# Kernel optimization log

Hardware: AMD Instinct MI355X
Metric: run time of the kernel (lower is better)

Reference implementation:

```python
import jax, jax.numpy as jnp
import numpy as np

DIM = 1024
HEADS = 16
HEAD_DIM = DIM // HEADS
SCALE = HEAD_DIM ** -0.5
HIDDEN = 4 * DIM
EPS = 1e-5


def _ln(x, g, b):
    m = jnp.mean(x, -1, keepdims=True)
    v = jnp.mean(jnp.square(x - m), -1, keepdims=True)
    return (x - m) / jnp.sqrt(v + EPS) * g + b


def _attn(x, wqkv, qb, vb, wp, bp):
    # x: (B, N, C). qkv bias = concat(q_bias, zeros, v_bias) as in the torch code.
    B, N, C = x.shape
    bias = jnp.concatenate([qb, jnp.zeros_like(vb), vb])
    qkv = (x @ wqkv.T + bias).reshape(B, N, 3, HEADS, HEAD_DIM).transpose(2, 0, 3, 1, 4)
    q, k, v = qkv[0], qkv[1], qkv[2]
    # qk_float=True: logits computed in float32
    logits = jnp.einsum('bhqd,bhkd->bhqk', (q * SCALE).astype(jnp.float32), k.astype(jnp.float32))
    a = jax.nn.softmax(logits, axis=-1).astype(x.dtype)
    o = jnp.einsum('bhqk,bhkd->bqhd', a, v).reshape(B, N, C)
    return o @ wp.T + bp


def setup_inputs() -> dict:
    key = jax.random.key(0)
    ks = jax.random.split(key, 16)
    s = 0.02
    d = {
        'x': jax.random.normal(ks[0], (4, 8, 196, DIM), jnp.float32),
        'cls_token': jax.random.normal(ks[1], (4, DIM), jnp.float32),
        # temporal branch
        'tln_g': jnp.ones((DIM,), jnp.float32), 'tln_b': jnp.zeros((DIM,), jnp.float32),
        't_wqkv': jax.random.normal(ks[2], (3 * DIM, DIM), jnp.float32) * s,
        't_qb': jax.random.normal(ks[3], (DIM,), jnp.float32) * s,
        't_vb': jax.random.normal(ks[4], (DIM,), jnp.float32) * s,
        't_wproj': jax.random.normal(ks[5], (DIM, DIM), jnp.float32) * s,
        't_bproj': jnp.zeros((DIM,), jnp.float32),
        't_fc_w': jax.random.normal(ks[6], (DIM, DIM), jnp.float32) * s,
        't_fc_b': jnp.zeros((DIM,), jnp.float32),
        # spatial branch
        'n1_g': jnp.ones((DIM,), jnp.float32), 'n1_b': jnp.zeros((DIM,), jnp.float32),
        's_wqkv': jax.random.normal(ks[7], (3 * DIM, DIM), jnp.float32) * s,
        's_qb': jax.random.normal(ks[8], (DIM,), jnp.float32) * s,
        's_vb': jax.random.normal(ks[9], (DIM,), jnp.float32) * s,
        's_wproj': jax.random.normal(ks[10], (DIM, DIM), jnp.float32) * s,
        's_bproj': jnp.zeros((DIM,), jnp.float32),
        # mlp
        'n2_g': jnp.ones((DIM,), jnp.float32), 'n2_b': jnp.zeros((DIM,), jnp.float32),
        'fc1_w': jax.random.normal(ks[11], (HIDDEN, DIM), jnp.float32) * s,
        'fc1_b': jnp.zeros((HIDDEN,), jnp.float32),
        'fc2_w': jax.random.normal(ks[12], (DIM, HIDDEN), jnp.float32) * s,
        'fc2_b': jnp.zeros((DIM,), jnp.float32),
    }
    return d


def reference(x, cls_token, tln_g, tln_b, t_wqkv, t_qb, t_vb, t_wproj, t_bproj,
              t_fc_w, t_fc_b, n1_g, n1_b, s_wqkv, s_qb, s_vb, s_wproj, s_bproj,
              n2_g, n2_b, fc1_w, fc1_b, fc2_w, fc2_b):
    B, T, N, C = x.shape
    # temporal attention: 'b t n m -> (b n) t m'
    xt = x.transpose(0, 2, 1, 3).reshape(B * N, T, C)
    xt = _attn(_ln(xt, tln_g, tln_b), t_wqkv, t_qb, t_vb, t_wproj, t_bproj)
    # '(b n) t m -> b (n t) m'
    xt = xt.reshape(B, N * T, C)
    xt = xt @ t_fc_w.T + t_fc_b
    xt = x.transpose(0, 2, 1, 3).reshape(B, N * T, C) + xt
    # spatial attention with cls token per frame
    init_cls = cls_token[:, None, :]                               # (B, 1, C)
    cls_rep = jnp.broadcast_to(init_cls, (B, T, C)).reshape(B * T, 1, C)
    xs = xt.reshape(B, N, T, C).transpose(0, 2, 1, 3).reshape(B * T, N, C)
    xs = jnp.concatenate([cls_rep, xs], axis=1)                    # (B*T, N+1, C)
    xs = _attn(_ln(xs, n1_g, n1_b), s_wqkv, s_qb, s_vb, s_wproj, s_bproj)
    cls_m = xs[:, 0, :].reshape(B, T, C).mean(axis=1, keepdims=True)  # (B, 1, C)
    xs = xs[:, 1:, :].reshape(B, T, N, C).transpose(0, 2, 1, 3).reshape(B, N * T, C)
    x2 = jnp.concatenate([init_cls, xt], axis=1) + jnp.concatenate([cls_m, xs], axis=1)
    # MLP (exact GELU, matching nn.GELU default)
    h = _ln(x2, n2_g, n2_b)
    h = jax.nn.gelu(h @ fc1_w.T + fc1_b, approximate=False) @ fc2_w.T + fc2_b
    x2 = x2 + h
    cls_out = x2[:, 0, :]
    xo = x2[:, 1:].reshape(B, N, T, C).transpose(0, 2, 1, 3)       # (B, T, N, C)
    return xo, cls_out
```

## Files before the change

kernel.cpp:

```cpp
#include <hip/hip_runtime.h>
#include <stdint.h>


#define SCALE 0.125f

typedef unsigned short u16;
typedef short bf16x8 __attribute__((ext_vector_type(8)));
typedef float f32x4 __attribute__((ext_vector_type(4)));

static constexpr int kNT    = 1568;
static constexpr int kRowsA = 6272;
static constexpr int kSeqS  = 197;
static constexpr int kRowsS = 6304;
static constexpr int kRowsC = 6276;
static constexpr size_t kXO = 6422528;

__device__ __forceinline__ float bf2f(u16 u) {
    union { unsigned int i; float f; } c; c.i = ((unsigned int)u) << 16; return c.f;
}
__device__ __forceinline__ u16 f2bf(float f) {
    union { float f; unsigned int i; } c; c.f = f;
    unsigned int r = c.i + 0x7FFFu + ((c.i >> 16) & 1u);
    return (u16)(r >> 16);
}

__device__ __forceinline__ void gll16(const void* g, void* l) {
    __builtin_amdgcn_global_load_lds((__attribute__((address_space(1))) void*)g,
                                     (__attribute__((address_space(3))) void*)l,
                                     16, 0, 0);
}

__global__ void convw_k(const float* __restrict__ in, u16* __restrict__ out, int n4) {
    const int stride = gridDim.x * blockDim.x;
    for (int i = blockIdx.x * blockDim.x + threadIdx.x; i < n4; i += stride) {
        float4 v = ((const float4*)in)[i];
        ushort4 o;
        o.x = f2bf(v.x); o.y = f2bf(v.y); o.z = f2bf(v.z); o.w = f2bf(v.w);
        ((ushort4*)out)[i] = o;
    }
}

__global__ void bias3_k(const float* __restrict__ qb, const float* __restrict__ vb,
                        float* __restrict__ dst) {
    const int i = blockIdx.x * 256 + threadIdx.x;
    if (i >= 3072) return;
    dst[i] = (i < 1024) ? qb[i] : (i < 2048) ? 0.0f : vb[i - 2048];
}

template<int MODE>
__global__ void ln_k(const float* __restrict__ src, const float* __restrict__ src2,
                     const float* __restrict__ g, const float* __restrict__ bt,
                     u16* __restrict__ out, int rows) {
    const int r = (blockIdx.x << 2) + (threadIdx.x >> 6);
    const int lane = threadIdx.x & 63;
    if (r >= rows) return;
    const float* srow;
    if constexpr (MODE == 0) {
        int b = r / kNT, rem = r - b * kNT, n = rem >> 3, t = rem & 7;
        srow = src + (((size_t)((b * 8 + t) * 196 + n)) << 10);
    } else if constexpr (MODE == 1) {
        int s2 = r / kSeqS, i = r - s2 * kSeqS, b = s2 >> 3, t = s2 & 7;
        srow = (i == 0) ? (src2 + ((size_t)b << 10))
                        : (src + (((size_t)(b * kNT + ((i - 1) << 3) + t)) << 10));
    } else {
        srow = src + ((size_t)r << 10);
    }
    float4 v[4]; float s = 0.f, ss = 0.f;
#pragma unroll
    for (int j = 0; j < 4; ++j) {
        v[j] = *(const float4*)&srow[((j << 6) + lane) << 2];
        s  += v[j].x + v[j].y + v[j].z + v[j].w;
        ss += v[j].x * v[j].x + v[j].y * v[j].y + v[j].z * v[j].z + v[j].w * v[j].w;
    }
#pragma unroll
    for (int off = 1; off < 64; off <<= 1) { s += __shfl_xor(s, off); ss += __shfl_xor(ss, off); }
    const float mean = s * (1.f / 1024.f);
    const float rstd = rsqrtf(ss * (1.f / 1024.f) - mean * mean + 1e-5f);
#pragma unroll
    for (int j = 0; j < 4; ++j) {
        const int c = ((j << 6) + lane) << 2;
        float4 gg = *(const float4*)&g[c];
        float4 bb = *(const float4*)&bt[c];
        ushort4 o;
        o.x = f2bf((v[j].x - mean) * rstd * gg.x + bb.x);
        o.y = f2bf((v[j].y - mean) * rstd * gg.y + bb.y);
        o.z = f2bf((v[j].z - mean) * rstd * gg.z + bb.z);
        o.w = f2bf((v[j].w - mean) * rstd * gg.w + bb.w);
        *(ushort4*)&out[((size_t)r << 10) + c] = o;
    }
}

template<int MODE, int TM>
__global__ __launch_bounds__(256, 4) void gemm_bt(
        const u16* __restrict__ A, const u16* __restrict__ W,
        const float* __restrict__ bias,
        u16* __restrict__ outB, float* __restrict__ outF,
        const float* __restrict__ resid, float* __restrict__ dout,
        int M, int N, int K) {
    constexpr int MF  = TM / 32;
    constexpr int NCA = TM / 64;
    __shared__ __align__(16) u16 As[2][TM * 32];
    __shared__ __align__(16) u16 Bs[2][128 * 32];
    const int tid  = threadIdx.x;
    const int lane = tid & 63, wave = tid >> 6;
    const int lo = lane & 15, hi = lane >> 4;
    const int wr = wave >> 1, wc = wave & 1;
    const int row0 = blockIdx.y * TM, col0 = blockIdx.x << 7;

    const u16* aP[NCA]; const u16* bP[2];
#pragma unroll
    for (int i = 0; i < NCA; ++i) {
        const int c = wave * TM + (i << 6) + lane;
        const int row = c >> 2;
        const int jl = (((c & 3) ^ (row & 3)) << 3);
        int ar = row0 + row; if (ar > M - 1) ar = M - 1;
        aP[i] = A + (size_t)ar * K + jl;
    }
#pragma unroll
    for (int i = 0; i < 2; ++i) {
        const int c = (wave << 7) + (i << 6) + lane;
        const int row = c >> 2;
        const int jl = (((c & 3) ^ (row & 3)) << 3);
        int br = col0 + row; if (br > N - 1) br = N - 1;
        bP[i] = W + (size_t)br * K + jl;
    }

    f32x4 acc[MF][4] = {};
    const int nk = K >> 5;

    auto stage = [&](int buf, int k0) {
#pragma unroll
        for (int i = 0; i < NCA; ++i)
            gll16(aP[i] + k0, &As[buf][wave * (TM * 8) + (i << 9)]);
#pragma unroll
        for (int i = 0; i < 2; ++i)
            gll16(bP[i] + k0, &Bs[buf][(wave << 10) + (i << 9)]);
    };

    stage(0, 0);
    __syncthreads();

    int cur = 0;
    for (int it = 0; it < nk; ++it) {
        const bool more = (it + 1) < nk;
        if (more) stage(cur ^ 1, (it + 1) << 5);
        const int sl = (hi ^ (lo & 3)) << 3;
        bf16x8 af[MF], bfr[4];
#pragma unroll
        for (int m = 0; m < MF; ++m)
            af[m] = *(const bf16x8*)&As[cur][((wr * (TM / 2) + (m << 4) + lo) << 5) + sl];
#pragma unroll
        for (int n = 0; n < 4; ++n)
            bfr[n] = *(const bf16x8*)&Bs[cur][(((wc << 6) + (n << 4) + lo) << 5) + sl];
#pragma unroll
        for (int m = 0; m < MF; ++m)
#pragma unroll
            for (int n = 0; n < 4; ++n)
                acc[m][n] = __builtin_amdgcn_mfma_f32_16x16x32_bf16(af[m], bfr[n], acc[m][n], 0, 0, 0);
        if (more) {
            __syncthreads();
            cur ^= 1;
        }
    }

#pragma unroll
    for (int m = 0; m < MF; ++m) {
        const int rb = row0 + wr * (TM / 2) + (m << 4) + (hi << 2);
#pragma unroll
        for (int n = 0; n < 4; ++n) {
            const int c = col0 + (wc << 6) + (n << 4) + lo;
            const float bc = bias[c];
#pragma unroll
            for (int j = 0; j < 4; ++j) {
                const int r = rb + j;
                if (r >= M) continue;
                float v = acc[m][n][j] + bc;
                if constexpr (MODE == 2) v = 0.5f * v * (1.0f + erff(v * 0.70710678f));
                if constexpr (MODE == 3) {
                    int b = r / 1568, rem = r - b * 1568, nn = rem >> 3, tt = rem & 7;
                    v += resid[(((size_t)((b * 8 + tt) * 196 + nn)) << 10) + c];
                }
                if constexpr (MODE == 0 || MODE == 2) {
                    outB[(size_t)r * N + c] = f2bf(v);
                } else if constexpr (MODE == 1 || MODE == 3) {
                    outF[(size_t)r * N + c] = v;
                } else {
                    v += resid[((size_t)r << 10) + c];
                    int b = r / 1569, i = r - b * 1569;
                    if (i == 0) dout[kXO + ((size_t)b << 10) + c] = v;
                    else {
                        int jj = i - 1, nn = jj >> 3, tt = jj & 7;
                        dout[(((size_t)((b * 8 + tt) * 196 + nn)) << 10) + c] = v;
                    }
                }
            }
        }
    }
}

__global__ void attn_a_k(const u16* __restrict__ qkv, u16* __restrict__ o) {
    __shared__ float lq[4][8][65], lk[4][8][65], lv[4][8][65];
    __shared__ float al[4][64];
    const int lane = threadIdx.x & 63, wave = threadIdx.x >> 6;
    const int p = (blockIdx.x << 2) + wave;
    const int s = p >> 4, h = p & 15;
    const u16* base = qkv + (size_t)s * 24576 + (h << 6);
    for (int u = lane; u < 1536; u += 64) {
        const int part = u >> 9, t = (u >> 6) & 7, d = u & 63;
        const float val = bf2f(base[(size_t)t * 3072 + (part << 10) + d]);
        if (part == 0) lq[wave][t][d] = val;
        else if (part == 1) lk[wave][t][d] = val;
        else lv[wave][t][d] = val;
    }
    __syncthreads();
    const int qi = lane >> 3, kj = lane & 7;
    float dot = 0.f;
#pragma unroll
    for (int d = 0; d < 64; ++d) dot += lq[wave][qi][d] * lk[wave][kj][d];
    dot *= SCALE;
    float m = dot;
    m = fmaxf(m, __shfl_xor(m, 1));
    m = fmaxf(m, __shfl_xor(m, 2));
    m = fmaxf(m, __shfl_xor(m, 4));
    const float e = expf(dot - m);
    float sm = e;
    sm += __shfl_xor(sm, 1);
    sm += __shfl_xor(sm, 2);
    sm += __shfl_xor(sm, 4);
    al[wave][lane] = e / sm;
    __syncthreads();
    u16* orow = o + (size_t)s * 8192 + (h << 6) + lane;
#pragma unroll
    for (int ii = 0; ii < 8; ++ii) {
        float accv = 0.f;
#pragma unroll
        for (int jj = 0; jj < 8; ++jj) accv += al[wave][(ii << 3) + jj] * lv[wave][jj][lane];
        orow[(size_t)ii * 1024] = f2bf(accv);
    }
}

__global__ __launch_bounds__(256, 2) void attn_s_mfma(const u16* __restrict__ qkv,
                                                      u16* __restrict__ o) {
    __shared__ __align__(16) u16 SM[29696];
    u16* __restrict__ Vt = SM;
    const int tid = threadIdx.x, lane = tid & 63, wave = tid >> 6;
    const int lo = lane & 15, hi = lane >> 4;
    u16* __restrict__ Pw = SM + 14848 + wave * 3712;
    const int s2 = blockIdx.x >> 4, h = blockIdx.x & 15;
    const u16* __restrict__ base = qkv + (size_t)s2 * (kSeqS * 3072) + (h << 6);

    for (int u = tid; u < 26 * 64; u += 256) {
        const int d = u & 63, k0 = (u >> 6) << 3;
        union { bf16x8 v; u16 e[8]; } pk;
#pragma unroll
        for (int i = 0; i < 8; ++i) {
            int kr = k0 + i; if (kr > 196) kr = 196;
            pk.e[i] = base[(size_t)kr * 3072 + 2048 + d];
        }
        *(bf16x8*)&Vt[d * 232 + k0] = pk.v;
    }
    for (int u = tid; u < 1024; u += 256)
        Vt[(u >> 4) * 232 + 208 + (u & 15)] = 0;
    for (int u = lane; u < 256; u += 64)
        Pw[(u >> 4) * 232 + 208 + (u & 15)] = 0;
    __syncthreads();

    for (int qt = wave; qt < 13; qt += 4) {
        int qr = qt * 16 + lo; if (qr > 196) qr = 196;
        const u16* qp = base + (size_t)qr * 3072;
        const bf16x8 aq0 = *(const bf16x8*)&qp[hi << 3];
        const bf16x8 aq1 = *(const bf16x8*)&qp[32 + (hi << 3)];

        f32x4 s[13];
#pragma unroll
        for (int kt = 0; kt < 13; ++kt) {
            int kr = kt * 16 + lo; if (kr > 196) kr = 196;
            const u16* kp = base + (size_t)kr * 3072 + 1024;
            const bf16x8 bk0 = *(const bf16x8*)&kp[hi << 3];
            const bf16x8 bk1 = *(const bf16x8*)&kp[32 + (hi << 3)];
            f32x4 acc = {};
            acc = __builtin_amdgcn_mfma_f32_16x16x32_bf16(aq0, bk0, acc, 0, 0, 0);
            acc = __builtin_amdgcn_mfma_f32_16x16x32_bf16(aq1, bk1, acc, 0, 0, 0);
            s[kt] = acc * SCALE;
        }
        if (lo > 4) s[12] = (f32x4){-1e30f, -1e30f, -1e30f, -1e30f};

        float inv[4];
#pragma unroll
        for (int j = 0; j < 4; ++j) {
            float m = s[0][j];
#pragma unroll
            for (int kt = 1; kt < 13; ++kt) m = fmaxf(m, s[kt][j]);
            m = fmaxf(m, __shfl_xor(m, 1));
            m = fmaxf(m, __shfl_xor(m, 2));
            m = fmaxf(m, __shfl_xor(m, 4));
            m = fmaxf(m, __shfl_xor(m, 8));
            float sum = 0.f;
#pragma unroll
            for (int kt = 0; kt < 13; ++kt) {
                const float e = __expf(s[kt][j] - m);
                s[kt][j] = e;
                sum += e;
            }
            sum += __shfl_xor(sum, 1);
            sum += __shfl_xor(sum, 2);
            sum += __shfl_xor(sum, 4);
            sum += __shfl_xor(sum, 8);
            inv[j] = 1.f / sum;
        }

#pragma unroll
        for (int kt = 0; kt < 13; ++kt)
#pragma unroll
            for (int j = 0; j < 4; ++j)
                Pw[((hi << 2) + j) * 232 + kt * 16 + lo] = f2bf(s[kt][j]);

        f32x4 o4[4] = {};
#pragma unroll
        for (int kc = 0; kc < 7; ++kc) {
            const bf16x8 pa = *(const bf16x8*)&Pw[lo * 232 + kc * 32 + (hi << 3)];
#pragma unroll
            for (int dt = 0; dt < 4; ++dt) {
                const bf16x8 vf = *(const bf16x8*)&Vt[(dt * 16 + lo) * 232 + kc * 32 + (hi << 3)];
                o4[dt] = __builtin_amdgcn_mfma_f32_16x16x32_bf16(pa, vf, o4[dt], 0, 0, 0);
            }
        }

#pragma unroll
        for (int j = 0; j < 4; ++j) {
            const int q = qt * 16 + (hi << 2) + j;
            if (q > 196) continue;
            u16* orow = o + (((size_t)(s2 * kSeqS + q)) << 10) + (h << 6);
#pragma unroll
            for (int dt = 0; dt < 4; ++dt)
                orow[dt * 16 + lo] = f2bf(o4[dt][j] * inv[j]);
        }
    }
}

__global__ void clsm_k(const float* __restrict__ xs, float* __restrict__ cm) {
    const int idx = blockIdx.x * 256 + threadIdx.x;
    if (idx >= 4096) return;
    const int b = idx >> 10, c = idx & 1023;
    float s = 0.f;
#pragma unroll
    for (int t = 0; t < 8; ++t) s += xs[(((size_t)(b * 8 + t)) * kSeqS) * 1024 + c];
    cm[idx] = s * 0.125f;
}

__global__ void build_x2_k(const float* __restrict__ xt, const float* __restrict__ xs,
                           const float* __restrict__ cls, const float* __restrict__ cm,
                           float* __restrict__ x2) {
    const int r = blockIdx.x;
    const int c = threadIdx.x << 2;
    const int b = r / 1569, i = r - b * 1569;
    const float* pa; const float* pb;
    if (i == 0) {
        pa = cls + ((size_t)b << 10) + c;
        pb = cm + ((size_t)b << 10) + c;
    } else {
        const int jj = i - 1, n = jj >> 3, t = jj & 7;
        pa = xt + (((size_t)(b * 1568 + jj)) << 10) + c;
        pb = xs + (((size_t)((b * 8 + t) * kSeqS + 1 + n)) << 10) + c;
    }
    const float4 va = *(const float4*)pa;
    const float4 vb = *(const float4*)pb;
    float4 vo;
    vo.x = va.x + vb.x; vo.y = va.y + vb.y; vo.z = va.z + vb.z; vo.w = va.w + vb.w;
    *(float4*)&x2[((size_t)r << 10) + c] = vo;
}

extern "C" void kernel_launch(void* const* d_in, const int* in_sizes, int n_in,
                              void* d_out, int out_size, void* d_ws, size_t ws_size,
                              hipStream_t stream) {
    const float* x       = (const float*)d_in[0];
    const float* cls     = (const float*)d_in[1];
    const float* tln_g   = (const float*)d_in[2];
    const float* tln_b   = (const float*)d_in[3];
    const float* t_wqkv  = (const float*)d_in[4];
    const float* t_qb    = (const float*)d_in[5];
    const float* t_vb    = (const float*)d_in[6];
    const float* t_wproj = (const float*)d_in[7];
    const float* t_bproj = (const float*)d_in[8];
    const float* t_fc_w  = (const float*)d_in[9];
    const float* t_fc_b  = (const float*)d_in[10];
    const float* n1_g    = (const float*)d_in[11];
    const float* n1_b    = (const float*)d_in[12];
    const float* s_wqkv  = (const float*)d_in[13];
    const float* s_qb    = (const float*)d_in[14];
    const float* s_vb    = (const float*)d_in[15];
    const float* s_wproj = (const float*)d_in[16];
    const float* s_bproj = (const float*)d_in[17];
    const float* n2_g    = (const float*)d_in[18];
    const float* n2_b    = (const float*)d_in[19];
    const float* fc1_w   = (const float*)d_in[20];
    const float* fc1_b   = (const float*)d_in[21];
    const float* fc2_w   = (const float*)d_in[22];
    const float* fc2_b   = (const float*)d_in[23];
    float* dout = (float*)d_out;
    char* ws = (char*)d_ws;

    size_t off = 0;
    auto alloc = [&](size_t bytes) { size_t o = off; off += (bytes + 255) & ~(size_t)255; return o; };

    u16* t_wqkv_bf  = (u16*)(ws + alloc(3145728ull * 2));
    u16* t_wproj_bf = (u16*)(ws + alloc(1048576ull * 2));
    u16* t_fcw_bf   = (u16*)(ws + alloc(1048576ull * 2));
    u16* s_wqkv_bf  = (u16*)(ws + alloc(3145728ull * 2));
    u16* s_wproj_bf = (u16*)(ws + alloc(1048576ull * 2));
    u16* fc1_bf     = (u16*)(ws + alloc(4194304ull * 2));
    u16* fc2_bf     = (u16*)(ws + alloc(4194304ull * 2));
    u16* ln_bf      = (u16*)(ws + alloc((size_t)kRowsS * 1024 * 2));
    u16* qkv_bf     = (u16*)(ws + alloc((size_t)kRowsS * 3072 * 2));
    u16* o_bf       = (u16*)(ws + alloc((size_t)kRowsS * 1024 * 2));
    u16* h1_bf      = qkv_bf;
    u16* mid_bf     = (u16*)(ws + alloc((size_t)kRowsA * 1024 * 2));
    float* xt_f     = (float*)(ws + alloc((size_t)kRowsA * 1024 * 4));
    float* xs_f     = (float*)(ws + alloc((size_t)kRowsS * 1024 * 4));
    float* x2_f     = (float*)(ws + alloc((size_t)kRowsC * 1024 * 4));
    float* bias_t   = (float*)(ws + alloc(3072 * 4));
    float* bias_s   = (float*)(ws + alloc(3072 * 4));
    float* clsm     = (float*)(ws + alloc(4096 * 4));
    (void)ws_size; (void)in_sizes; (void)n_in; (void)out_size;

    convw_k<<<dim3(1024), dim3(256), 0, stream>>>(t_wqkv, t_wqkv_bf, 786432);
    convw_k<<<dim3(512),  dim3(256), 0, stream>>>(t_wproj, t_wproj_bf, 262144);
    convw_k<<<dim3(512),  dim3(256), 0, stream>>>(t_fc_w, t_fcw_bf, 262144);
    convw_k<<<dim3(1024), dim3(256), 0, stream>>>(s_wqkv, s_wqkv_bf, 786432);
    convw_k<<<dim3(512),  dim3(256), 0, stream>>>(s_wproj, s_wproj_bf, 262144);
    convw_k<<<dim3(1024), dim3(256), 0, stream>>>(fc1_w, fc1_bf, 1048576);
    convw_k<<<dim3(1024), dim3(256), 0, stream>>>(fc2_w, fc2_bf, 1048576);
    bias3_k<<<dim3(12), dim3(256), 0, stream>>>(t_qb, t_vb, bias_t);
    bias3_k<<<dim3(12), dim3(256), 0, stream>>>(s_qb, s_vb, bias_s);

    ln_k<0><<<dim3(kRowsA / 4), dim3(256), 0, stream>>>(x, nullptr, tln_g, tln_b, ln_bf, kRowsA);
    gemm_bt<0, 128><<<dim3(24, 49), dim3(256), 0, stream>>>(ln_bf, t_wqkv_bf, bias_t, qkv_bf, nullptr, nullptr, nullptr, kRowsA, 3072, 1024);
    attn_a_k<<<dim3(3136), dim3(256), 0, stream>>>(qkv_bf, o_bf);
    gemm_bt<0, 64><<<dim3(8, 98), dim3(256), 0, stream>>>(o_bf, t_wproj_bf, t_bproj, mid_bf, nullptr, nullptr, nullptr, kRowsA, 1024, 1024);
    gemm_bt<3, 64><<<dim3(8, 98), dim3(256), 0, stream>>>(mid_bf, t_fcw_bf, t_fc_b, nullptr, xt_f, x, nullptr, kRowsA, 1024, 1024);

    ln_k<1><<<dim3(kRowsS / 4), dim3(256), 0, stream>>>(xt_f, cls, n1_g, n1_b, ln_bf, kRowsS);
    gemm_bt<0, 128><<<dim3(24, 50), dim3(256), 0, stream>>>(ln_bf, s_wqkv_bf, bias_s, qkv_bf, nullptr, nullptr, nullptr, kRowsS, 3072, 1024);
    attn_s_mfma<<<dim3(512), dim3(256), 0, stream>>>(qkv_bf, o_bf);
    gemm_bt<1, 64><<<dim3(8, 99), dim3(256), 0, stream>>>(o_bf, s_wproj_bf, s_bproj, nullptr, xs_f, nullptr, nullptr, kRowsS, 1024, 1024);
    clsm_k<<<dim3(16), dim3(256), 0, stream>>>(xs_f, clsm);
    build_x2_k<<<dim3(kRowsC), dim3(256), 0, stream>>>(xt_f, xs_f, cls, clsm, x2_f);

    ln_k<2><<<dim3(kRowsC / 4), dim3(256), 0, stream>>>(x2_f, nullptr, n2_g, n2_b, ln_bf, kRowsC);
    gemm_bt<2, 128><<<dim3(32, 50), dim3(256), 0, stream>>>(ln_bf, fc1_bf, fc1_b, h1_bf, nullptr, nullptr, nullptr, kRowsC, 4096, 1024);
    gemm_bt<4, 64><<<dim3(8, 99), dim3(256), 0, stream>>>(h1_bf, fc2_bf, fc2_b, nullptr, nullptr, x2_f, dout, kRowsC, 1024, 4096);
}
```

Baseline: 553.8 us.

## Fold temporal proj and fc weights, single-buffer GEMM, retile fc2

Precomputes a combined weight t_fc_w @ t_wproj (via a transpose and a small GEMM) and a combined bias, so the temporal branch runs one 1024x1024 GEMM instead of two back-to-back GEMMs and drops an intermediate activation buffer. The GEMM kernel also changes from double-buffered LDS staging to a single buffer with two barriers per k-step, drops launch_bounds, and uses a different LDS swizzle. The fc2 GEMM switches to 128-row tiles. Folding the weights changes rounding, since the intermediate activation is no longer rounded to bf16. Losing the double buffering may expose global-load latency in every GEMM.

```diff
diff --git a/kernel.cpp b/kernel.cpp
--- a/kernel.cpp
+++ b/kernel.cpp
@@ -38,6 +38,28 @@
         o.x = f2bf(v.x); o.y = f2bf(v.y); o.z = f2bf(v.z); o.w = f2bf(v.w);
         ((ushort4*)out)[i] = o;
     }
+}
+
+__global__ void transpose_bf_k(const float* __restrict__ in, u16* __restrict__ out) {
+    __shared__ float t[16][17];
+    const int tx = threadIdx.x & 15, ty = threadIdx.x >> 4;
+    const int bx = blockIdx.x, by = blockIdx.y;
+    t[ty][tx] = in[(size_t)(by * 16 + ty) * 1024 + bx * 16 + tx];
+    __syncthreads();
+    out[(size_t)(bx * 16 + ty) * 1024 + by * 16 + tx] = f2bf(t[tx][ty]);
+}
+
+__global__ void bcomb_k(const float* __restrict__ fcw, const float* __restrict__ bp,
+                        const float* __restrict__ fcb, float* __restrict__ out) {
+    const int row = blockIdx.x * 4 + (threadIdx.x >> 6);
+    const int lane = threadIdx.x & 63;
+    float s = 0.f;
+#pragma unroll
+    for (int i = 0; i < 16; ++i)
+        s += fcw[(size_t)row * 1024 + (i << 6) + lane] * bp[(i << 6) + lane];
+#pragma unroll
+    for (int off = 1; off < 64; off <<= 1) s += __shfl_xor(s, off);
+    if (lane == 0) out[row] = s + fcb[row];
 }
 
 __global__ void bias3_k(const float* __restrict__ qb, const float* __restrict__ vb,
@@ -91,7 +113,7 @@
 }
 
 template<int MODE, int TM>
-__global__ __launch_bounds__(256, 4) void gemm_bt(
+__global__ void gemm_bt(
         const u16* __restrict__ A, const u16* __restrict__ W,
         const float* __restrict__ bias,
         u16* __restrict__ outB, float* __restrict__ outF,
@@ -99,8 +121,8 @@
         int M, int N, int K) {
     constexpr int MF  = TM / 32;
     constexpr int NCA = TM / 64;
-    __shared__ __align__(16) u16 As[2][TM * 32];
-    __shared__ __align__(16) u16 Bs[2][128 * 32];
+    __shared__ __align__(16) u16 As[TM * 32];
+    __shared__ __align__(16) u16 Bs[128 * 32];
     const int tid  = threadIdx.x;
     const int lane = tid & 63, wave = tid >> 6;
     const int lo = lane & 15, hi = lane >> 4;
@@ -112,7 +134,7 @@
     for (int i = 0; i < NCA; ++i) {
         const int c = wave * TM + (i << 6) + lane;
         const int row = c >> 2;
-        const int jl = (((c & 3) ^ (row & 3)) << 3);
+        const int jl = (((c & 3) ^ ((c >> 3) & 3)) << 3);
         int ar = row0 + row; if (ar > M - 1) ar = M - 1;
         aP[i] = A + (size_t)ar * K + jl;
     }
@@ -120,47 +142,35 @@
     for (int i = 0; i < 2; ++i) {
         const int c = (wave << 7) + (i << 6) + lane;
         const int row = c >> 2;
-        const int jl = (((c & 3) ^ (row & 3)) << 3);
+        const int jl = (((c & 3) ^ ((c >> 3) & 3)) << 3);
         int br = col0 + row; if (br > N - 1) br = N - 1;
         bP[i] = W + (size_t)br * K + jl;
     }
 
     f32x4 acc[MF][4] = {};
-    const int nk = K >> 5;
-
-    auto stage = [&](int buf, int k0) {
+    const int sl = (hi ^ ((lo >> 1) & 3)) << 3;
+
+    for (int k0 = 0; k0 < K; k0 += 32) {
 #pragma unroll
         for (int i = 0; i < NCA; ++i)
-            gll16(aP[i] + k0, &As[buf][wave * (TM * 8) + (i << 9)]);
+            gll16(aP[i] + k0, &As[wave * (TM * 8) + (i << 9)]);
 #pragma unroll
         for (int i = 0; i < 2; ++i)
-            gll16(bP[i] + k0, &Bs[buf][(wave << 10) + (i << 9)]);
-    };
-
-    stage(0, 0);
-    __syncthreads();
-
-    int cur = 0;
-    for (int it = 0; it < nk; ++it) {
-        const bool more = (it + 1) < nk;
-        if (more) stage(cur ^ 1, (it + 1) << 5);
-        const int sl = (hi ^ (lo & 3)) << 3;
+            gll16(bP[i] + k0, &Bs[(wave << 10) + (i << 9)]);
+        __syncthreads();
         bf16x8 af[MF], bfr[4];
 #pragma unroll
         for (int m = 0; m < MF; ++m)
-            af[m] = *(const bf16x8*)&As[cur][((wr * (TM / 2) + (m << 4) + lo) << 5) + sl];
+            af[m] = *(const bf16x8*)&As[((wr * (TM / 2) + (m << 4) + lo) << 5) + sl];
 #pragma unroll
         for (int n = 0; n < 4; ++n)
-            bfr[n] = *(const bf16x8*)&Bs[cur][(((wc << 6) + (n << 4) + lo) << 5) + sl];
+            bfr[n] = *(const bf16x8*)&Bs[(((wc << 6) + (n << 4) + lo) << 5) + sl];
 #pragma unroll
         for (int m = 0; m < MF; ++m)
 #pragma unroll
             for (int n = 0; n < 4; ++n)
                 acc[m][n] = __builtin_amdgcn_mfma_f32_16x16x32_bf16(af[m], bfr[n], acc[m][n], 0, 0, 0);
-        if (more) {
-            __syncthreads();
-            cur ^= 1;
-        }
+        __syncthreads();
     }
 
 #pragma unroll
@@ -404,7 +414,7 @@
     auto alloc = [&](size_t bytes) { size_t o = off; off += (bytes + 255) & ~(size_t)255; return o; };
 
     u16* t_wqkv_bf  = (u16*)(ws + alloc(3145728ull * 2));
-    u16* t_wproj_bf = (u16*)(ws + alloc(1048576ull * 2));
+    u16* wpT_bf     = (u16*)(ws + alloc(1048576ull * 2));
     u16* t_fcw_bf   = (u16*)(ws + alloc(1048576ull * 2));
     u16* s_wqkv_bf  = (u16*)(ws + alloc(3145728ull * 2));
     u16* s_wproj_bf = (u16*)(ws + alloc(1048576ull * 2));
@@ -414,17 +424,17 @@
     u16* qkv_bf     = (u16*)(ws + alloc((size_t)kRowsS * 3072 * 2));
     u16* o_bf       = (u16*)(ws + alloc((size_t)kRowsS * 1024 * 2));
     u16* h1_bf      = qkv_bf;
-    u16* mid_bf     = (u16*)(ws + alloc((size_t)kRowsA * 1024 * 2));
+    u16* wcomb_bf   = (u16*)(ws + alloc(1048576ull * 2));
     float* xt_f     = (float*)(ws + alloc((size_t)kRowsA * 1024 * 4));
     float* xs_f     = (float*)(ws + alloc((size_t)kRowsS * 1024 * 4));
     float* x2_f     = (float*)(ws + alloc((size_t)kRowsC * 1024 * 4));
     float* bias_t   = (float*)(ws + alloc(3072 * 4));
     float* bias_s   = (float*)(ws + alloc(3072 * 4));
     float* clsm     = (float*)(ws + alloc(4096 * 4));
+    float* bcomb    = (float*)(ws + alloc(1024 * 4));
     (void)ws_size; (void)in_sizes; (void)n_in; (void)out_size;
 
     convw_k<<<dim3(1024), dim3(256), 0, stream>>>(t_wqkv, t_wqkv_bf, 786432);
-    convw_k<<<dim3(512),  dim3(256), 0, stream>>>(t_wproj, t_wproj_bf, 262144);
     convw_k<<<dim3(512),  dim3(256), 0, stream>>>(t_fc_w, t_fcw_bf, 262144);
     convw_k<<<dim3(1024), dim3(256), 0, stream>>>(s_wqkv, s_wqkv_bf, 786432);
     convw_k<<<dim3(512),  dim3(256), 0, stream>>>(s_wproj, s_wproj_bf, 262144);
@@ -432,12 +442,15 @@
     convw_k<<<dim3(1024), dim3(256), 0, stream>>>(fc2_w, fc2_bf, 1048576);
     bias3_k<<<dim3(12), dim3(256), 0, stream>>>(t_qb, t_vb, bias_t);
     bias3_k<<<dim3(12), dim3(256), 0, stream>>>(s_qb, s_vb, bias_s);
+    transpose_bf_k<<<dim3(64, 64), dim3(256), 0, stream>>>(t_wproj, wpT_bf);
+    bcomb_k<<<dim3(256), dim3(256), 0, stream>>>(t_fc_w, t_bproj, t_fc_b, bcomb);
+    gemm_bt<0, 128><<<dim3(8, 8), dim3(256), 0, stream>>>(
+        t_fcw_bf, wpT_bf, bias_t + 1024, wcomb_bf, nullptr, nullptr, nullptr, 1024, 1024, 1024);
 
     ln_k<0><<<dim3(kRowsA / 4), dim3(256), 0, stream>>>(x, nullptr, tln_g, tln_b, ln_bf, kRowsA);
     gemm_bt<0, 128><<<dim3(24, 49), dim3(256), 0, stream>>>(ln_bf, t_wqkv_bf, bias_t, qkv_bf, nullptr, nullptr, nullptr, kRowsA, 3072, 1024);
     attn_a_k<<<dim3(3136), dim3(256), 0, stream>>>(qkv_bf, o_bf);
-    gemm_bt<0, 64><<<dim3(8, 98), dim3(256), 0, stream>>>(o_bf, t_wproj_bf, t_bproj, mid_bf, nullptr, nullptr, nullptr, kRowsA, 1024, 1024);
-    gemm_bt<3, 64><<<dim3(8, 98), dim3(256), 0, stream>>>(mid_bf, t_fcw_bf, t_fc_b, nullptr, xt_f, x, nullptr, kRowsA, 1024, 1024);
+    gemm_bt<3, 64><<<dim3(8, 98), dim3(256), 0, stream>>>(o_bf, wcomb_bf, bcomb, nullptr, xt_f, x, nullptr, kRowsA, 1024, 1024);
 
     ln_k<1><<<dim3(kRowsS / 4), dim3(256), 0, stream>>>(xt_f, cls, n1_g, n1_b, ln_bf, kRowsS);
     gemm_bt<0, 128><<<dim3(24, 50), dim3(256), 0, stream>>>(ln_bf, s_wqkv_bf, bias_s, qkv_bf, nullptr, nullptr, nullptr, kRowsS, 3072, 1024);
@@ -448,5 +461,5 @@
 
     ln_k<2><<<dim3(kRowsC / 4), dim3(256), 0, stream>>>(x2_f, nullptr, n2_g, n2_b, ln_bf, kRowsC);
     gemm_bt<2, 128><<<dim3(32, 50), dim3(256), 0, stream>>>(ln_bf, fc1_bf, fc1_b, h1_bf, nullptr, nullptr, nullptr, kRowsC, 4096, 1024);
-    gemm_bt<4, 64><<<dim3(8, 99), dim3(256), 0, stream>>>(h1_bf, fc2_bf, fc2_b, nullptr, nullptr, x2_f, dout, kRowsC, 1024, 4096);
-}
+    gemm_bt<4, 128><<<dim3(8, 50), dim3(256), 0, stream>>>(h1_bf, fc2_bf, fc2_b, nullptr, nullptr, x2_f, dout, kRowsC, 1024, 4096);
+}
```

After: 533.6 us. 3.7% less time.
